# Optimization experiments

Measured on AMD Instinct MI355X. Metric: run time of the kernel, lower is better.

The kernel has to match this reference:

```python
import jax, jax.numpy as jnp
import numpy as np

N = 262144   # number of units (batched instances of the module)
G = 128      # universe_field side length
D = 128      # dimension
RADIUS = 3   # min(3, G//2) == 3

# First D=128 neighborhood offsets in the original triple-loop order (i-major, j, k)
_grid = np.stack(np.meshgrid(np.arange(-RADIUS, RADIUS + 1),
                             np.arange(-RADIUS, RADIUS + 1),
                             np.arange(-RADIUS, RADIUS + 1), indexing='ij'), -1).reshape(-1, 3)[:D]
OI = jnp.asarray(_grid[:, 0], dtype=jnp.int32)
OJ = jnp.asarray(_grid[:, 1], dtype=jnp.int32)
OK = jnp.asarray(_grid[:, 2], dtype=jnp.int32)


def setup_inputs() -> dict:
    key = jax.random.key(0)
    ks = jax.random.split(key, 8)
    return {
        'universe_field': jax.random.normal(ks[0], (G, G, G), jnp.float32),
        'positions': jax.random.uniform(ks[1], (N, 3), jnp.float32) * G,
        'signatures': jax.random.normal(ks[2], (N, D), jnp.float32),
        'offsets': jax.random.normal(ks[3], (N, 3), jnp.float32) * 0.1,
        'W1': jax.random.normal(ks[4], (2 * D, D), jnp.float32) * (1.0 / np.sqrt(2 * D)),
        'b1': jax.random.normal(ks[5], (D,), jnp.float32) * 0.01,
        'W2': jax.random.normal(ks[6], (D, D), jnp.float32) * (1.0 / np.sqrt(D)),
        'b2': jax.random.normal(ks[7], (D,), jnp.float32) * 0.01,
    }


def _sample_local(field, pos):
    # pos: [N,3] float; truncate to int (torch .long()) then clamp, like the original
    pc = jnp.clip(jax.lax.stop_gradient(pos).astype(jnp.int32), 0, G - 1)  # [N,3]
    xx = jnp.clip(pc[:, 0:1] + OI[None, :], 0, G - 1)  # [N,D]
    yy = jnp.clip(pc[:, 1:2] + OJ[None, :], 0, G - 1)
    zz = jnp.clip(pc[:, 2:3] + OK[None, :], 0, G - 1)
    return field[xx, yy, zz]  # [N,D] gathered local field (343 points truncated to D)


def _stability(field, pos, signatures, W1, b1, W2, b2):
    local = _sample_local(field, pos)                       # [N,D]
    combined = jnp.concatenate([signatures, local], axis=-1)  # [N,2D]
    h = jnp.tanh(combined @ W1 + b1)                        # [N,D]
    resp = h @ W2 + b2                                      # [N,D]
    return jnp.linalg.norm(resp - signatures, axis=-1)      # [N]


def reference(universe_field, positions, signatures, offsets, W1, b1, W2, b2):
    stab_old = _stability(universe_field, positions, signatures, W1, b1, W2, b2)
    test_pos = positions + offsets
    stab_new = _stability(universe_field, test_pos, signatures, W1, b1, W2, b2)
    accept = stab_new <= stab_old                           # revert move if new_stab > old_stab
    final_pos = jnp.where(accept[:, None], test_pos, positions)
    stability = jnp.where(accept, stab_new, stab_old)
    return stability, final_pos
```

## Files before the change

kernel.cpp:

```cpp
#include <hip/hip_runtime.h>
#include <hip/hip_bf16.h>

#define NU 262144
#define GG 128
#define PG 134
#define DD 128

typedef __attribute__((ext_vector_type(8))) short short8;
typedef __attribute__((ext_vector_type(4))) float f32x4;

union Frag { short8 s; unsigned u[4]; };

__device__ __forceinline__ unsigned short f2b(float f) {
  union { float f; unsigned u; } v; v.f = f;
  unsigned r = v.u + 0x7fffu + ((v.u >> 16) & 1u);
  return (unsigned short)(r >> 16);
}
__device__ __forceinline__ unsigned cvtpk(float lo, float hi) {
  unsigned r;
  asm("v_cvt_pk_bf16_f32 %0, %1, %2" : "=v"(r) : "v"(lo), "v"(hi));
  return r;
}

__device__ __forceinline__ float fast_tanh(float x) {
  float ax = fabsf(x);
  float e  = __expf(ax + ax);
  float t  = 1.0f - __fdividef(2.0f, e + 1.0f);
  return copysignf(t, x);
}

struct alignas(16) RowdT { int v[20]; };
static constexpr RowdT mkrowd() {
  RowdT t{};
  for (int r = 0; r < 20; ++r) {
    int rr = (r < 18) ? r : 18;
    int di = (rr < 18) ? (-3 + rr / 7) : -1;
    int dj = (rr < 18) ? (-3 + rr % 7) : 1;
    t.v[r] = (di * PG + dj) * PG - 3;
  }
  return t;
}
__device__ constexpr RowdT ROWD = mkrowd();

__global__ void prep_field(const float* __restrict__ f, unsigned short* __restrict__ fp) {
  int idx = blockIdx.x * 256 + threadIdx.x;
  if (idx >= PG * PG * PG) return;
  int z = idx % PG, t = idx / PG;
  int y = t % PG, x = t / PG;
  int xx = min(max(x - 3, 0), GG - 1);
  int yy = min(max(y - 3, 0), GG - 1);
  int zz = min(max(z - 3, 0), GG - 1);
  fp[idx] = f2b(f[(xx * GG + yy) * GG + zz]);
}

__global__ void prep_w(const float* __restrict__ W1, const float* __restrict__ W2,
                       unsigned short* __restrict__ wall) {
  int idx = blockIdx.x * 256 + threadIdx.x;
  if (idx >= 6656) return;
  int kt = idx >> 9, nt = (idx >> 6) & 7, ln = idx & 63;
  int n = nt * 16 + (ln & 15), lg = ln >> 4;
  short8 s;
  if (kt < 4) {
    int k0 = kt * 32 + lg * 8;
#pragma unroll
    for (int j = 0; j < 8; ++j) s[j] = (short)f2b(W1[(k0 + j) * DD + n]);
  } else if (kt < 9) {
    int r = (kt - 4) * 4 + lg;
#pragma unroll
    for (int j = 0; j < 8; ++j) {
      bool valid = (r < 18 && j < 7) || (r == 18 && j < 2);
      int row = 128 + ((r < 18) ? (r * 7 + j) : (126 + j));
      s[j] = valid ? (short)f2b(W1[row * DD + n]) : (short)0;
    }
  } else {
    int k0 = (kt - 9) * 32 + lg * 8;
#pragma unroll
    for (int j = 0; j < 8; ++j) s[j] = (short)f2b(W2[(k0 + j) * DD + n]);
  }
  ((short8*)wall)[idx] = s;
}

__global__ __launch_bounds__(512, 4) void atu_main(
    const float* __restrict__ pos, const float* __restrict__ sig,
    const float* __restrict__ offs,
    const float* __restrict__ b1, const float* __restrict__ b2,
    const unsigned short* __restrict__ fpad, const unsigned short* __restrict__ wall,
    float* __restrict__ out_stab, float* __restrict__ out_pos)
{
  __shared__ unsigned short ldsw[2][8192];
  const int tid  = threadIdx.x;
  const int lane = tid & 63;
  const int lg   = lane >> 4, lm = lane & 15;
  const int wid  = tid >> 6;
  int bid = blockIdx.x;
  int swz = (bid & 7) * 256 + (bid >> 3);
  const int ub = swz * 128 + wid * 16;
  const int un = ub + lm;

  int abase[2];
  {
    float px = pos[un * 3 + 0], py = pos[un * 3 + 1], pz = pos[un * 3 + 2];
    float qx = px + offs[un * 3 + 0], qy = py + offs[un * 3 + 1], qz = pz + offs[un * 3 + 2];
    int ax = min(max((int)px, 0), GG - 1), ay = min(max((int)py, 0), GG - 1), az = min(max((int)pz, 0), GG - 1);
    int bx = min(max((int)qx, 0), GG - 1), by = min(max((int)qy, 0), GG - 1), bz = min(max((int)qz, 0), GG - 1);
    abase[0] = ((ax + 3) * PG + (ay + 3)) * PG + (az + 3);
    abase[1] = ((bx + 3) * PG + (by + 3)) * PG + (bz + 3);
  }

  const short8* wfr = (const short8*)wall;
  const char* fpadb = (const char*)fpad;

  f32x4 acc[8][2];
#pragma unroll
  for (int nt = 0; nt < 8; ++nt) { acc[nt][0] = f32x4{0.f,0.f,0.f,0.f}; acc[nt][1] = f32x4{0.f,0.f,0.f,0.f}; }
  f32x4 acc2[8][2];
  unsigned Q[2][8][2];

#define WRBUF(H, R0, R1)                                                        \
  *(short8*)((char*)&ldsw[H][0] + tid * 16) = (R0);                             \
  *(short8*)((char*)&ldsw[H][0] + 8192 + tid * 16) = (R1);

#define SIG_KT(KT, HALF)                                                        \
  {                                                                             \
    const f32x4* sp = (const f32x4*)(sig + (size_t)un * DD + (KT) * 32 + lg * 8); \
    f32x4 a = sp[0], b = sp[1];                                                 \
    Frag B;                                                                     \
    B.u[0] = cvtpk(a[0], a[1]); B.u[1] = cvtpk(a[2], a[3]);                     \
    B.u[2] = cvtpk(b[0], b[1]); B.u[3] = cvtpk(b[2], b[3]);                     \
    const char* buf = (const char*)&ldsw[HALF][0] + (((KT) & 1) ? 8192 : 0);    \
    __builtin_amdgcn_s_setprio(1);                                              \
    _Pragma("unroll")                                                           \
    for (int nt = 0; nt < 8; ++nt) {                                            \
      short8 af = *(const short8*)(buf + (nt * 64 + lane) * 16);                \
      acc[nt][0] = __builtin_amdgcn_mfma_f32_16x16x32_bf16(af, B.s, acc[nt][0], 0, 0, 0); \
    }                                                                           \
    __builtin_amdgcn_s_setprio(0);                                              \
  }

#define ROW_KT(KT, HALF)                                                        \
  {                                                                             \
    int rd = ROWD.v[((KT) - 4) * 4 + lg];                                       \
    short8 B0 = *(const short8*)(fpadb + 2 * (size_t)(abase[0] + rd));          \
    short8 B1 = *(const short8*)(fpadb + 2 * (size_t)(abase[1] + rd));          \
    const char* buf = (const char*)&ldsw[HALF][0] + (((KT) & 1) ? 8192 : 0);    \
    __builtin_amdgcn_s_setprio(1);                                              \
    _Pragma("unroll")                                                           \
    for (int nt = 0; nt < 8; ++nt) {                                            \
      short8 af = *(const short8*)(buf + (nt * 64 + lane) * 16);                \
      acc[nt][0] = __builtin_amdgcn_mfma_f32_16x16x32_bf16(af, B0, acc[nt][0], 0, 0, 0); \
      acc[nt][1] = __builtin_amdgcn_mfma_f32_16x16x32_bf16(af, B1, acc[nt][1], 0, 0, 0); \
    }                                                                           \
    __builtin_amdgcn_s_setprio(0);                                              \
  }

#define G2_KT(KT, HALF)                                                         \
  {                                                                             \
    constexpr int kb = (KT) - 9;                                                \
    Frag W[2];                                                                  \
    _Pragma("unroll")                                                           \
    for (int ut = 0; ut < 2; ++ut) {                                            \
      int qa0 = (int)Q[ut][2 * kb][0],     qa1 = (int)Q[ut][2 * kb][1];         \
      int qb0 = (int)Q[ut][2 * kb + 1][0], qb1 = (int)Q[ut][2 * kb + 1][1];     \
      int r00 = __builtin_amdgcn_ds_bpermute(ad0, qa0);                         \
      int r01 = __builtin_amdgcn_ds_bpermute(ad0, qa1);                         \
      int r10 = __builtin_amdgcn_ds_bpermute(ad1, qa0);                         \
      int r11 = __builtin_amdgcn_ds_bpermute(ad1, qa1);                         \
      int s00 = __builtin_amdgcn_ds_bpermute(ad0, qb0);                         \
      int s01 = __builtin_amdgcn_ds_bpermute(ad0, qb1);                         \
      int s10 = __builtin_amdgcn_ds_bpermute(ad1, qb0);                         \
      int s11 = __builtin_amdgcn_ds_bpermute(ad1, qb1);                         \
      W[ut].u[0] = (unsigned)(hi ? s00 : r00);                                  \
      W[ut].u[1] = (unsigned)(hi ? s01 : r01);                                  \
      W[ut].u[2] = (unsigned)(hi ? s10 : r10);                                  \
      W[ut].u[3] = (unsigned)(hi ? s11 : r11);                                  \
    }                                                                           \
    const char* buf = (const char*)&ldsw[HALF][0] + (((KT) & 1) ? 8192 : 0);    \
    __builtin_amdgcn_s_setprio(1);                                              \
    _Pragma("unroll")                                                           \
    for (int nt = 0; nt < 8; ++nt) {                                            \
      short8 af = *(const short8*)(buf + (nt * 64 + lane) * 16);                \
      acc2[nt][0] = __builtin_amdgcn_mfma_f32_16x16x32_bf16(af, W[0].s, acc2[nt][0], 0, 0, 0); \
      acc2[nt][1] = __builtin_amdgcn_mfma_f32_16x16x32_bf16(af, W[1].s, acc2[nt][1], 0, 0, 0); \
    }                                                                           \
    __builtin_amdgcn_s_setprio(0);                                              \
  }

  const int ad0 = ((((2 * lg) & 3) * 16) + lm) * 4;
  const int ad1 = ((((2 * lg + 1) & 3) * 16) + lm) * 4;
  const bool hi = (lg >= 2);

  short8 c0 = wfr[tid],        c1 = wfr[512 + tid];
  short8 n0 = wfr[1024 + tid], n1 = wfr[1536 + tid];
  WRBUF(0, c0, c1)
  __syncthreads();

  c0 = wfr[2048 + tid]; c1 = wfr[2560 + tid];
  SIG_KT(0, 0) SIG_KT(1, 0)
  WRBUF(1, n0, n1)
  __syncthreads();

  n0 = wfr[3072 + tid]; n1 = wfr[3584 + tid];
  SIG_KT(2, 1) SIG_KT(3, 1)
  WRBUF(0, c0, c1)
  __syncthreads();

#pragma unroll
  for (int nt = 0; nt < 8; ++nt) acc[nt][1] = acc[nt][0];

  c0 = wfr[4096 + tid]; c1 = wfr[4608 + tid];
  ROW_KT(4, 0) ROW_KT(5, 0)
  WRBUF(1, n0, n1)
  __syncthreads();

  n0 = wfr[5120 + tid]; n1 = wfr[5632 + tid];
  ROW_KT(6, 1) ROW_KT(7, 1)
  WRBUF(0, c0, c1)
  __syncthreads();

  c0 = wfr[6144 + tid];
  ROW_KT(8, 0)

#pragma unroll
  for (int nt = 0; nt < 8; ++nt) {
    f32x4 b1v = *(const f32x4*)(b1 + nt * 16 + lg * 4);
#pragma unroll
    for (int ut = 0; ut < 2; ++ut) {
      float h0 = fast_tanh(acc[nt][ut][0] + b1v[0]);
      float h1 = fast_tanh(acc[nt][ut][1] + b1v[1]);
      float h2 = fast_tanh(acc[nt][ut][2] + b1v[2]);
      float h3 = fast_tanh(acc[nt][ut][3] + b1v[3]);
      Q[ut][nt][0] = cvtpk(h0, h1);
      Q[ut][nt][1] = cvtpk(h2, h3);
    }
  }
#pragma unroll
  for (int nt = 0; nt < 8; ++nt) {
    f32x4 b2v = *(const f32x4*)(b2 + nt * 16 + lg * 4);
    acc2[nt][0] = b2v; acc2[nt][1] = b2v;
  }

  G2_KT(9, 0)
  WRBUF(1, n0, n1)
  __syncthreads();

  G2_KT(10, 1) G2_KT(11, 1)
  *(short8*)((char*)&ldsw[0][0] + tid * 16) = c0;
  __syncthreads();

  G2_KT(12, 0)

  float ssq[2] = {0.f, 0.f};
#pragma unroll
  for (int nt = 0; nt < 8; ++nt) {
    f32x4 sv = *(const f32x4*)(sig + (size_t)un * DD + nt * 16 + lg * 4);
#pragma unroll
    for (int ut = 0; ut < 2; ++ut) {
#pragma unroll
      for (int r = 0; r < 4; ++r) {
        float d = acc2[nt][ut][r] - sv[r];
        ssq[ut] = fmaf(d, d, ssq[ut]);
      }
    }
  }
  ssq[0] += __shfl_xor(ssq[0], 16, 64); ssq[0] += __shfl_xor(ssq[0], 32, 64);
  ssq[1] += __shfl_xor(ssq[1], 16, 64); ssq[1] += __shfl_xor(ssq[1], 32, 64);

  if (lane < 16) {
    float px = pos[un * 3 + 0], py = pos[un * 3 + 1], pz = pos[un * 3 + 2];
    float ox = offs[un * 3 + 0], oy = offs[un * 3 + 1], oz = offs[un * 3 + 2];
    bool ok = ssq[1] <= ssq[0];
    out_stab[un] = sqrtf(ok ? ssq[1] : ssq[0]);
    out_pos[un * 3 + 0] = ok ? px + ox : px;
    out_pos[un * 3 + 1] = ok ? py + oy : py;
    out_pos[un * 3 + 2] = ok ? pz + oz : pz;
  }
#undef WRBUF
#undef SIG_KT
#undef ROW_KT
#undef G2_KT
}

extern "C" void kernel_launch(void* const* d_in, const int* in_sizes, int n_in,
                              void* d_out, int out_size, void* d_ws, size_t ws_size,
                              hipStream_t stream) {
  const float* field = (const float*)d_in[0];
  const float* pos   = (const float*)d_in[1];
  const float* sig   = (const float*)d_in[2];
  const float* offs  = (const float*)d_in[3];
  const float* W1    = (const float*)d_in[4];
  const float* b1    = (const float*)d_in[5];
  const float* W2    = (const float*)d_in[6];
  const float* b2    = (const float*)d_in[7];
  float* out_stab = (float*)d_out;
  float* out_pos  = out_stab + NU;

  char* ws = (char*)d_ws;
  unsigned short* fpad = (unsigned short*)ws;
  unsigned short* wall = (unsigned short*)(ws + 4812800);

  prep_field<<<(PG * PG * PG + 255) / 256, 256, 0, stream>>>(field, fpad);
  prep_w<<<26, 256, 0, stream>>>(W1, W2, wall);
  atu_main<<<NU / 128, 512, 0, stream>>>(pos, sig, offs, b1, b2,
                                         fpad, wall, out_stab, out_pos);
}
```

Before: 149.6 us.

## Process 32 units per wave and preload all W1 tiles into LDS

```diff
diff --git a/kernel.cpp b/kernel.cpp
--- a/kernel.cpp
+++ b/kernel.cpp
@@ -80,204 +80,185 @@
   ((short8*)wall)[idx] = s;
 }
 
-__global__ __launch_bounds__(512, 4) void atu_main(
+__global__ __launch_bounds__(512, 2) void atu_main(
     const float* __restrict__ pos, const float* __restrict__ sig,
     const float* __restrict__ offs,
     const float* __restrict__ b1, const float* __restrict__ b2,
     const unsigned short* __restrict__ fpad, const unsigned short* __restrict__ wall,
     float* __restrict__ out_stab, float* __restrict__ out_pos)
 {
-  __shared__ unsigned short ldsw[2][8192];
+  __shared__ unsigned short ldsw[9 * 4096];
   const int tid  = threadIdx.x;
   const int lane = tid & 63;
   const int lg   = lane >> 4, lm = lane & 15;
   const int wid  = tid >> 6;
   int bid = blockIdx.x;
-  int swz = (bid & 7) * 256 + (bid >> 3);
-  const int ub = swz * 128 + wid * 16;
-  const int un = ub + lm;
-
-  int abase[2];
-  {
-    float px = pos[un * 3 + 0], py = pos[un * 3 + 1], pz = pos[un * 3 + 2];
-    float qx = px + offs[un * 3 + 0], qy = py + offs[un * 3 + 1], qz = pz + offs[un * 3 + 2];
+  int swz = (bid & 7) * 128 + (bid >> 3);
+  const int ub  = swz * 256 + wid * 32;
+  const int un0 = ub + lm, un1 = ub + 16 + lm;
+
+  short8* lds8 = (short8*)ldsw;
+  const short8* wfr = (const short8*)wall;
+
+#pragma unroll
+  for (int i = 0; i < 9; ++i) lds8[i * 512 + tid] = wfr[i * 512 + tid];
+
+  int abase[4];
+#pragma unroll
+  for (int ug = 0; ug < 2; ++ug) {
+    int u = ub + ug * 16 + lm;
+    float px = pos[u * 3 + 0], py = pos[u * 3 + 1], pz = pos[u * 3 + 2];
+    float qx = px + offs[u * 3 + 0], qy = py + offs[u * 3 + 1], qz = pz + offs[u * 3 + 2];
     int ax = min(max((int)px, 0), GG - 1), ay = min(max((int)py, 0), GG - 1), az = min(max((int)pz, 0), GG - 1);
     int bx = min(max((int)qx, 0), GG - 1), by = min(max((int)qy, 0), GG - 1), bz = min(max((int)qz, 0), GG - 1);
-    abase[0] = ((ax + 3) * PG + (ay + 3)) * PG + (az + 3);
-    abase[1] = ((bx + 3) * PG + (by + 3)) * PG + (bz + 3);
-  }
-
-  const short8* wfr = (const short8*)wall;
+    abase[ug]     = ((ax + 3) * PG + (ay + 3)) * PG + (az + 3);
+    abase[2 + ug] = ((bx + 3) * PG + (by + 3)) * PG + (bz + 3);
+  }
+  __syncthreads();
+
+  f32x4 acc[8][4];
+#pragma unroll
+  for (int nt = 0; nt < 8; ++nt)
+#pragma unroll
+    for (int s = 0; s < 4; ++s) acc[nt][s] = f32x4{0.f, 0.f, 0.f, 0.f};
+
+#pragma unroll
+  for (int kt = 0; kt < 4; ++kt) {
+    Frag B[2];
+#pragma unroll
+    for (int ug = 0; ug < 2; ++ug) {
+      const f32x4* sp = (const f32x4*)(sig + (size_t)(ub + ug * 16 + lm) * DD + kt * 32 + lg * 8);
+      f32x4 a = sp[0], b = sp[1];
+      B[ug].u[0] = cvtpk(a[0], a[1]); B[ug].u[1] = cvtpk(a[2], a[3]);
+      B[ug].u[2] = cvtpk(b[0], b[1]); B[ug].u[3] = cvtpk(b[2], b[3]);
+    }
+    const char* buf = (const char*)ldsw + kt * 8192;
+#pragma unroll
+    for (int nt = 0; nt < 8; ++nt) {
+      short8 af = *(const short8*)(buf + (nt * 64 + lane) * 16);
+      acc[nt][0] = __builtin_amdgcn_mfma_f32_16x16x32_bf16(af, B[0].s, acc[nt][0], 0, 0, 0);
+      acc[nt][1] = __builtin_amdgcn_mfma_f32_16x16x32_bf16(af, B[1].s, acc[nt][1], 0, 0, 0);
+    }
+  }
+#pragma unroll
+  for (int nt = 0; nt < 8; ++nt) { acc[nt][2] = acc[nt][0]; acc[nt][3] = acc[nt][1]; }
+
   const char* fpadb = (const char*)fpad;
-
-  f32x4 acc[8][2];
-#pragma unroll
-  for (int nt = 0; nt < 8; ++nt) { acc[nt][0] = f32x4{0.f,0.f,0.f,0.f}; acc[nt][1] = f32x4{0.f,0.f,0.f,0.f}; }
-  f32x4 acc2[8][2];
-  unsigned Q[2][8][2];
-
-#define WRBUF(H, R0, R1)                                                        \
-  *(short8*)((char*)&ldsw[H][0] + tid * 16) = (R0);                             \
-  *(short8*)((char*)&ldsw[H][0] + 8192 + tid * 16) = (R1);
-
-#define SIG_KT(KT, HALF)                                                        \
-  {                                                                             \
-    const f32x4* sp = (const f32x4*)(sig + (size_t)un * DD + (KT) * 32 + lg * 8); \
-    f32x4 a = sp[0], b = sp[1];                                                 \
-    Frag B;                                                                     \
-    B.u[0] = cvtpk(a[0], a[1]); B.u[1] = cvtpk(a[2], a[3]);                     \
-    B.u[2] = cvtpk(b[0], b[1]); B.u[3] = cvtpk(b[2], b[3]);                     \
-    const char* buf = (const char*)&ldsw[HALF][0] + (((KT) & 1) ? 8192 : 0);    \
-    __builtin_amdgcn_s_setprio(1);                                              \
-    _Pragma("unroll")                                                           \
-    for (int nt = 0; nt < 8; ++nt) {                                            \
-      short8 af = *(const short8*)(buf + (nt * 64 + lane) * 16);                \
-      acc[nt][0] = __builtin_amdgcn_mfma_f32_16x16x32_bf16(af, B.s, acc[nt][0], 0, 0, 0); \
-    }                                                                           \
-    __builtin_amdgcn_s_setprio(0);                                              \
-  }
-
-#define ROW_KT(KT, HALF)                                                        \
-  {                                                                             \
-    int rd = ROWD.v[((KT) - 4) * 4 + lg];                                       \
-    short8 B0 = *(const short8*)(fpadb + 2 * (size_t)(abase[0] + rd));          \
-    short8 B1 = *(const short8*)(fpadb + 2 * (size_t)(abase[1] + rd));          \
-    const char* buf = (const char*)&ldsw[HALF][0] + (((KT) & 1) ? 8192 : 0);    \
-    __builtin_amdgcn_s_setprio(1);                                              \
-    _Pragma("unroll")                                                           \
-    for (int nt = 0; nt < 8; ++nt) {                                            \
-      short8 af = *(const short8*)(buf + (nt * 64 + lane) * 16);                \
-      acc[nt][0] = __builtin_amdgcn_mfma_f32_16x16x32_bf16(af, B0, acc[nt][0], 0, 0, 0); \
-      acc[nt][1] = __builtin_amdgcn_mfma_f32_16x16x32_bf16(af, B1, acc[nt][1], 0, 0, 0); \
-    }                                                                           \
-    __builtin_amdgcn_s_setprio(0);                                              \
-  }
-
-#define G2_KT(KT, HALF)                                                         \
-  {                                                                             \
-    constexpr int kb = (KT) - 9;                                                \
-    Frag W[2];                                                                  \
-    _Pragma("unroll")                                                           \
-    for (int ut = 0; ut < 2; ++ut) {                                            \
-      int qa0 = (int)Q[ut][2 * kb][0],     qa1 = (int)Q[ut][2 * kb][1];         \
-      int qb0 = (int)Q[ut][2 * kb + 1][0], qb1 = (int)Q[ut][2 * kb + 1][1];     \
-      int r00 = __builtin_amdgcn_ds_bpermute(ad0, qa0);                         \
-      int r01 = __builtin_amdgcn_ds_bpermute(ad0, qa1);                         \
-      int r10 = __builtin_amdgcn_ds_bpermute(ad1, qa0);                         \
-      int r11 = __builtin_amdgcn_ds_bpermute(ad1, qa1);                         \
-      int s00 = __builtin_amdgcn_ds_bpermute(ad0, qb0);                         \
-      int s01 = __builtin_amdgcn_ds_bpermute(ad0, qb1);                         \
-      int s10 = __builtin_amdgcn_ds_bpermute(ad1, qb0);                         \
-      int s11 = __builtin_amdgcn_ds_bpermute(ad1, qb1);                         \
-      W[ut].u[0] = (unsigned)(hi ? s00 : r00);                                  \
-      W[ut].u[1] = (unsigned)(hi ? s01 : r01);                                  \
-      W[ut].u[2] = (unsigned)(hi ? s10 : r10);                                  \
-      W[ut].u[3] = (unsigned)(hi ? s11 : r11);                                  \
-    }                                                                           \
-    const char* buf = (const char*)&ldsw[HALF][0] + (((KT) & 1) ? 8192 : 0);    \
-    __builtin_amdgcn_s_setprio(1);                                              \
-    _Pragma("unroll")                                                           \
-    for (int nt = 0; nt < 8; ++nt) {                                            \
-      short8 af = *(const short8*)(buf + (nt * 64 + lane) * 16);                \
-      acc2[nt][0] = __builtin_amdgcn_mfma_f32_16x16x32_bf16(af, W[0].s, acc2[nt][0], 0, 0, 0); \
-      acc2[nt][1] = __builtin_amdgcn_mfma_f32_16x16x32_bf16(af, W[1].s, acc2[nt][1], 0, 0, 0); \
-    }                                                                           \
-    __builtin_amdgcn_s_setprio(0);                                              \
+#pragma unroll
+  for (int kt = 4; kt < 9; ++kt) {
+    int rd = ROWD.v[(kt - 4) * 4 + lg];
+    short8 B[4];
+#pragma unroll
+    for (int s = 0; s < 4; ++s)
+      B[s] = *(const short8*)(fpadb + 2 * (size_t)(abase[s] + rd));
+    const char* buf = (const char*)ldsw + kt * 8192;
+#pragma unroll
+    for (int nt = 0; nt < 8; ++nt) {
+      short8 af = *(const short8*)(buf + (nt * 64 + lane) * 16);
+#pragma unroll
+      for (int s = 0; s < 4; ++s)
+        acc[nt][s] = __builtin_amdgcn_mfma_f32_16x16x32_bf16(af, B[s], acc[nt][s], 0, 0, 0);
+    }
   }
 
   const int ad0 = ((((2 * lg) & 3) * 16) + lm) * 4;
   const int ad1 = ((((2 * lg + 1) & 3) * 16) + lm) * 4;
   const bool hi = (lg >= 2);
-
-  short8 c0 = wfr[tid],        c1 = wfr[512 + tid];
-  short8 n0 = wfr[1024 + tid], n1 = wfr[1536 + tid];
-  WRBUF(0, c0, c1)
+  Frag Wt[4][4];
+#pragma unroll
+  for (int kb = 0; kb < 4; ++kb) {
+    f32x4 b1a = *(const f32x4*)(b1 + (2 * kb) * 16 + lg * 4);
+    f32x4 b1b = *(const f32x4*)(b1 + (2 * kb + 1) * 16 + lg * 4);
+#pragma unroll
+    for (int s = 0; s < 4; ++s) {
+      float a0 = fast_tanh(acc[2 * kb][s][0] + b1a[0]);
+      float a1 = fast_tanh(acc[2 * kb][s][1] + b1a[1]);
+      float a2 = fast_tanh(acc[2 * kb][s][2] + b1a[2]);
+      float a3 = fast_tanh(acc[2 * kb][s][3] + b1a[3]);
+      float c0 = fast_tanh(acc[2 * kb + 1][s][0] + b1b[0]);
+      float c1 = fast_tanh(acc[2 * kb + 1][s][1] + b1b[1]);
+      float c2 = fast_tanh(acc[2 * kb + 1][s][2] + b1b[2]);
+      float c3 = fast_tanh(acc[2 * kb + 1][s][3] + b1b[3]);
+      int qa0 = (int)cvtpk(a0, a1), qa1 = (int)cvtpk(a2, a3);
+      int qb0 = (int)cvtpk(c0, c1), qb1 = (int)cvtpk(c2, c3);
+      int r00 = __builtin_amdgcn_ds_bpermute(ad0, qa0);
+      int r01 = __builtin_amdgcn_ds_bpermute(ad0, qa1);
+      int r10 = __builtin_amdgcn_ds_bpermute(ad1, qa0);
+      int r11 = __builtin_amdgcn_ds_bpermute(ad1, qa1);
+      int s00 = __builtin_amdgcn_ds_bpermute(ad0, qb0);
+      int s01 = __builtin_amdgcn_ds_bpermute(ad0, qb1);
+      int s10 = __builtin_amdgcn_ds_bpermute(ad1, qb0);
+      int s11 = __builtin_amdgcn_ds_bpermute(ad1, qb1);
+      Wt[s][kb].u[0] = (unsigned)(hi ? s00 : r00);
+      Wt[s][kb].u[1] = (unsigned)(hi ? s01 : r01);
+      Wt[s][kb].u[2] = (unsigned)(hi ? s10 : r10);
+      Wt[s][kb].u[3] = (unsigned)(hi ? s11 : r11);
+    }
+  }
+
   __syncthreads();
-
-  c0 = wfr[2048 + tid]; c1 = wfr[2560 + tid];
-  SIG_KT(0, 0) SIG_KT(1, 0)
-  WRBUF(1, n0, n1)
+#pragma unroll
+  for (int i = 0; i < 4; ++i) lds8[i * 512 + tid] = wfr[(9 + i) * 512 + tid];
   __syncthreads();
 
-  n0 = wfr[3072 + tid]; n1 = wfr[3584 + tid];
-  SIG_KT(2, 1) SIG_KT(3, 1)
-  WRBUF(0, c0, c1)
-  __syncthreads();
-
-#pragma unroll
-  for (int nt = 0; nt < 8; ++nt) acc[nt][1] = acc[nt][0];
-
-  c0 = wfr[4096 + tid]; c1 = wfr[4608 + tid];
-  ROW_KT(4, 0) ROW_KT(5, 0)
-  WRBUF(1, n0, n1)
-  __syncthreads();
-
-  n0 = wfr[5120 + tid]; n1 = wfr[5632 + tid];
-  ROW_KT(6, 1) ROW_KT(7, 1)
-  WRBUF(0, c0, c1)
-  __syncthreads();
-
-  c0 = wfr[6144 + tid];
-  ROW_KT(8, 0)
-
-#pragma unroll
-  for (int nt = 0; nt < 8; ++nt) {
-    f32x4 b1v = *(const f32x4*)(b1 + nt * 16 + lg * 4);
-#pragma unroll
-    for (int ut = 0; ut < 2; ++ut) {
-      float h0 = fast_tanh(acc[nt][ut][0] + b1v[0]);
-      float h1 = fast_tanh(acc[nt][ut][1] + b1v[1]);
-      float h2 = fast_tanh(acc[nt][ut][2] + b1v[2]);
-      float h3 = fast_tanh(acc[nt][ut][3] + b1v[3]);
-      Q[ut][nt][0] = cvtpk(h0, h1);
-      Q[ut][nt][1] = cvtpk(h2, h3);
-    }
-  }
-#pragma unroll
-  for (int nt = 0; nt < 8; ++nt) {
-    f32x4 b2v = *(const f32x4*)(b2 + nt * 16 + lg * 4);
-    acc2[nt][0] = b2v; acc2[nt][1] = b2v;
-  }
-
-  G2_KT(9, 0)
-  WRBUF(1, n0, n1)
-  __syncthreads();
-
-  G2_KT(10, 1) G2_KT(11, 1)
-  *(short8*)((char*)&ldsw[0][0] + tid * 16) = c0;
-  __syncthreads();
-
-  G2_KT(12, 0)
-
-  float ssq[2] = {0.f, 0.f};
-#pragma unroll
-  for (int nt = 0; nt < 8; ++nt) {
-    f32x4 sv = *(const f32x4*)(sig + (size_t)un * DD + nt * 16 + lg * 4);
-#pragma unroll
-    for (int ut = 0; ut < 2; ++ut) {
-#pragma unroll
-      for (int r = 0; r < 4; ++r) {
-        float d = acc2[nt][ut][r] - sv[r];
-        ssq[ut] = fmaf(d, d, ssq[ut]);
+  float ssq[4] = {0.f, 0.f, 0.f, 0.f};
+#pragma unroll 1
+  for (int half = 0; half < 2; ++half) {
+    f32x4 acc2[4][4];
+#pragma unroll
+    for (int n2 = 0; n2 < 4; ++n2) {
+      f32x4 b2v = *(const f32x4*)(b2 + (half * 4 + n2) * 16 + lg * 4);
+#pragma unroll
+      for (int s = 0; s < 4; ++s) acc2[n2][s] = b2v;
+    }
+#pragma unroll
+    for (int kt = 0; kt < 4; ++kt) {
+      const char* buf = (const char*)ldsw + kt * 8192;
+#pragma unroll
+      for (int n2 = 0; n2 < 4; ++n2) {
+        int nt = half * 4 + n2;
+        short8 af = *(const short8*)(buf + (nt * 64 + lane) * 16);
+#pragma unroll
+        for (int s = 0; s < 4; ++s)
+          acc2[n2][s] = __builtin_amdgcn_mfma_f32_16x16x32_bf16(af, Wt[s][kt].s, acc2[n2][s], 0, 0, 0);
       }
     }
-  }
-  ssq[0] += __shfl_xor(ssq[0], 16, 64); ssq[0] += __shfl_xor(ssq[0], 32, 64);
-  ssq[1] += __shfl_xor(ssq[1], 16, 64); ssq[1] += __shfl_xor(ssq[1], 32, 64);
-
-  if (lane < 16) {
+#pragma unroll
+    for (int n2 = 0; n2 < 4; ++n2) {
+      int nt = half * 4 + n2;
+      f32x4 sv0 = *(const f32x4*)(sig + (size_t)un0 * DD + nt * 16 + lg * 4);
+      f32x4 sv1 = *(const f32x4*)(sig + (size_t)un1 * DD + nt * 16 + lg * 4);
+#pragma unroll
+      for (int s = 0; s < 4; ++s) {
+        f32x4 sv = (s & 1) ? sv1 : sv0;
+#pragma unroll
+        for (int r = 0; r < 4; ++r) {
+          float d = acc2[n2][s][r] - sv[r];
+          ssq[s] = fmaf(d, d, ssq[s]);
+        }
+      }
+    }
+  }
+
+#pragma unroll
+  for (int s = 0; s < 4; ++s) {
+    ssq[s] += __shfl_xor(ssq[s], 16, 64);
+    ssq[s] += __shfl_xor(ssq[s], 32, 64);
+  }
+
+  if (lane < 32) {
+    bool g1 = (lane >= 16);
+    float e0 = g1 ? ssq[1] : ssq[0];
+    float e1 = g1 ? ssq[3] : ssq[2];
+    int un = ub + (lane & 31);
     float px = pos[un * 3 + 0], py = pos[un * 3 + 1], pz = pos[un * 3 + 2];
     float ox = offs[un * 3 + 0], oy = offs[un * 3 + 1], oz = offs[un * 3 + 2];
-    bool ok = ssq[1] <= ssq[0];
-    out_stab[un] = sqrtf(ok ? ssq[1] : ssq[0]);
+    bool ok = e1 <= e0;
+    out_stab[un] = sqrtf(ok ? e1 : e0);
     out_pos[un * 3 + 0] = ok ? px + ox : px;
     out_pos[un * 3 + 1] = ok ? py + oy : py;
     out_pos[un * 3 + 2] = ok ? pz + oz : pz;
   }
-#undef WRBUF
-#undef SIG_KT
-#undef ROW_KT
-#undef G2_KT
 }
 
 extern "C" void kernel_launch(void* const* d_in, const int* in_sizes, int n_in,
@@ -300,6 +281,6 @@
 
   prep_field<<<(PG * PG * PG + 255) / 256, 256, 0, stream>>>(field, fpad);
   prep_w<<<26, 256, 0, stream>>>(W1, W2, wall);
-  atu_main<<<NU / 128, 512, 0, stream>>>(pos, sig, offs, b1, b2,
+  atu_main<<<NU / 256, 512, 0, stream>>>(pos, sig, offs, b1, b2,
                                          fpad, wall, out_stab, out_pos);
 }
```

Result: slower. 160.2 us (+7.0%).

## Cache bf16 signatures in LDS for residual, drop setprio, use rcp tanh

Applied to the files above, without the earlier changes.

```diff
diff --git a/kernel.cpp b/kernel.cpp
--- a/kernel.cpp
+++ b/kernel.cpp
@@ -21,12 +21,17 @@
   asm("v_cvt_pk_bf16_f32 %0, %1, %2" : "=v"(r) : "v"(lo), "v"(hi));
   return r;
 }
+__device__ __forceinline__ float unplo(unsigned w) {
+  union { unsigned u; float f; } v; v.u = w << 16; return v.f;
+}
+__device__ __forceinline__ float unphi(unsigned w) {
+  union { unsigned u; float f; } v; v.u = w & 0xffff0000u; return v.f;
+}
 
 __device__ __forceinline__ float fast_tanh(float x) {
-  float ax = fabsf(x);
-  float e  = __expf(ax + ax);
-  float t  = 1.0f - __fdividef(2.0f, e + 1.0f);
-  return copysignf(t, x);
+  float e = __expf(fabsf(x) * 2.0f);
+  float r = __frcp_rn(e + 1.0f);
+  return copysignf(fmaf(-2.0f, r, 1.0f), x);
 }
 
 struct alignas(16) RowdT { int v[20]; };
@@ -88,6 +93,7 @@
     float* __restrict__ out_stab, float* __restrict__ out_pos)
 {
   __shared__ unsigned short ldsw[2][8192];
+  __shared__ alignas(16) unsigned short ns[8][2048];
   const int tid  = threadIdx.x;
   const int lane = tid & 63;
   const int lg   = lane >> 4, lm = lane & 15;
@@ -96,6 +102,7 @@
   int swz = (bid & 7) * 256 + (bid >> 3);
   const int ub = swz * 128 + wid * 16;
   const int un = ub + lm;
+  char* nsb = (char*)&ns[wid][0];
 
   int abase[2];
   {
@@ -127,14 +134,14 @@
     Frag B;                                                                     \
     B.u[0] = cvtpk(a[0], a[1]); B.u[1] = cvtpk(a[2], a[3]);                     \
     B.u[2] = cvtpk(b[0], b[1]); B.u[3] = cvtpk(b[2], b[3]);                     \
+     \
+    *(short8*)(nsb + ((KT) * 4 + lg) * 256 + lm * 16) = B.s;                    \
     const char* buf = (const char*)&ldsw[HALF][0] + (((KT) & 1) ? 8192 : 0);    \
-    __builtin_amdgcn_s_setprio(1);                                              \
     _Pragma("unroll")                                                           \
     for (int nt = 0; nt < 8; ++nt) {                                            \
       short8 af = *(const short8*)(buf + (nt * 64 + lane) * 16);                \
       acc[nt][0] = __builtin_amdgcn_mfma_f32_16x16x32_bf16(af, B.s, acc[nt][0], 0, 0, 0); \
     }                                                                           \
-    __builtin_amdgcn_s_setprio(0);                                              \
   }
 
 #define ROW_KT(KT, HALF)                                                        \
@@ -143,14 +150,12 @@
     short8 B0 = *(const short8*)(fpadb + 2 * (size_t)(abase[0] + rd));          \
     short8 B1 = *(const short8*)(fpadb + 2 * (size_t)(abase[1] + rd));          \
     const char* buf = (const char*)&ldsw[HALF][0] + (((KT) & 1) ? 8192 : 0);    \
-    __builtin_amdgcn_s_setprio(1);                                              \
     _Pragma("unroll")                                                           \
     for (int nt = 0; nt < 8; ++nt) {                                            \
       short8 af = *(const short8*)(buf + (nt * 64 + lane) * 16);                \
       acc[nt][0] = __builtin_amdgcn_mfma_f32_16x16x32_bf16(af, B0, acc[nt][0], 0, 0, 0); \
       acc[nt][1] = __builtin_amdgcn_mfma_f32_16x16x32_bf16(af, B1, acc[nt][1], 0, 0, 0); \
     }                                                                           \
-    __builtin_amdgcn_s_setprio(0);                                              \
   }
 
 #define G2_KT(KT, HALF)                                                         \
@@ -175,14 +180,12 @@
       W[ut].u[3] = (unsigned)(hi ? s11 : r11);                                  \
     }                                                                           \
     const char* buf = (const char*)&ldsw[HALF][0] + (((KT) & 1) ? 8192 : 0);    \
-    __builtin_amdgcn_s_setprio(1);                                              \
     _Pragma("unroll")                                                           \
     for (int nt = 0; nt < 8; ++nt) {                                            \
       short8 af = *(const short8*)(buf + (nt * 64 + lane) * 16);                \
       acc2[nt][0] = __builtin_amdgcn_mfma_f32_16x16x32_bf16(af, W[0].s, acc2[nt][0], 0, 0, 0); \
       acc2[nt][1] = __builtin_amdgcn_mfma_f32_16x16x32_bf16(af, W[1].s, acc2[nt][1], 0, 0, 0); \
     }                                                                           \
-    __builtin_amdgcn_s_setprio(0);                                              \
   }
 
   const int ad0 = ((((2 * lg) & 3) * 16) + lm) * 4;
@@ -252,14 +255,21 @@
   float ssq[2] = {0.f, 0.f};
 #pragma unroll
   for (int nt = 0; nt < 8; ++nt) {
-    f32x4 sv = *(const f32x4*)(sig + (size_t)un * DD + nt * 16 + lg * 4);
+    unsigned long long w64 = *(const unsigned long long*)
+        (nsb + (nt * 2 + (lg >> 1)) * 256 + lm * 16 + (lg & 1) * 8);
+    unsigned w0 = (unsigned)w64, w1 = (unsigned)(w64 >> 32);
+    float sv0 = unplo(w0), sv1 = unphi(w0);
+    float sv2 = unplo(w1), sv3 = unphi(w1);
 #pragma unroll
     for (int ut = 0; ut < 2; ++ut) {
-#pragma unroll
-      for (int r = 0; r < 4; ++r) {
-        float d = acc2[nt][ut][r] - sv[r];
-        ssq[ut] = fmaf(d, d, ssq[ut]);
-      }
+      float d0 = acc2[nt][ut][0] - sv0;
+      float d1 = acc2[nt][ut][1] - sv1;
+      float d2 = acc2[nt][ut][2] - sv2;
+      float d3 = acc2[nt][ut][3] - sv3;
+      ssq[ut] = fmaf(d0, d0, ssq[ut]);
+      ssq[ut] = fmaf(d1, d1, ssq[ut]);
+      ssq[ut] = fmaf(d2, d2, ssq[ut]);
+      ssq[ut] = fmaf(d3, d3, ssq[ut]);
     }
   }
   ssq[0] += __shfl_xor(ssq[0], 16, 64); ssq[0] += __shfl_xor(ssq[0], 32, 64);
```

Result: no change. 147.0 us (-1.8%).
